# Kernel tuning notes

Hardware: AMD Instinct MI355X
Metric: run time of the kernel (lower is better)

Reference implementation:

```python
import jax, jax.numpy as jnp
import numpy as np
from functools import partial
from jax import lax

B, K, CLIP_DIM, SBERT_DIM, D_MODEL, R_RANK, ATTN_DIM, PMAX = 128, 1024, 768, 384, 256, 64, 256, 8
RHO = 0.35

def _normalize(x, axis=-1, eps=1e-12):
    return x / jnp.maximum(jnp.linalg.norm(x, axis=axis, keepdims=True), eps)

def _build_graph():
    rng = np.random.default_rng(0)
    pid = np.zeros((K, PMAX), np.int32)
    pm = np.zeros((K, PMAX), bool)
    for i in range(K - 1):  # node i's parents are in (i, K); root = K-1 has none
        n = int(rng.integers(1, PMAX + 1))
        n = min(n, K - 1 - i)
        cands = rng.choice(np.arange(i + 1, K), size=n, replace=False)
        pid[i, :n] = cands
        pm[i, :n] = True
    order = np.arange(K - 1, -1, -1, dtype=np.int32)  # parents before children
    return jnp.asarray(pid), jnp.asarray(pm), jnp.asarray(order)

def setup_inputs() -> dict:
    key = jax.random.key(0)
    ks = iter(jax.random.split(key, 32))
    r = lambda shape, s=0.02: jax.random.normal(next(ks), shape, jnp.float32) * s
    pid, pm, order = _build_graph()
    return {
        "t_clip": jax.random.normal(next(ks), (B, CLIP_DIM), jnp.float32),
        "v_clip": jax.random.normal(next(ks), (B, CLIP_DIM), jnp.float32),
        "concept_sbert": jax.random.normal(next(ks), (K, SBERT_DIM), jnp.float32),
        "Wt": r((CLIP_DIM, D_MODEL)), "bt": jnp.zeros((D_MODEL,)),
        "Wv": r((CLIP_DIM, D_MODEL)), "bv": jnp.zeros((D_MODEL,)),
        "Wc": r((SBERT_DIM, D_MODEL)), "bc": jnp.zeros((D_MODEL,)),
        "Wp1": r((3 * D_MODEL, 2 * D_MODEL)), "bp1": jnp.zeros((2 * D_MODEL,)),
        "Wp2": r((2 * D_MODEL, D_MODEL)), "bp2": jnp.zeros((D_MODEL,)),
        "Wm1": r((3 * D_MODEL, 2 * D_MODEL)), "bm1": jnp.zeros((2 * D_MODEL,)),
        "Wm2": r((2 * D_MODEL, D_MODEL)), "bm2": jnp.zeros((D_MODEL,)),
        "tau_logits": jnp.zeros((K,)),
        "U": r((D_MODEL, R_RANK)), "V": r((D_MODEL, R_RANK)),
        "Wg1": r((SBERT_DIM, R_RANK)), "bg1": jnp.zeros((R_RANK,)),
        "Wg2": r((R_RANK, R_RANK)), "bg2": jnp.zeros((R_RANK,)),
        "w_out": r((K, R_RANK)), "b_out": jnp.zeros((K,)),
        "concept_q": r((K, ATTN_DIM)),
        "parents_idx": pid, "parents_mask": pm, "order": order,
    }

def _forward(t_clip, v_clip, concept_sbert, Wt, bt, Wv, bv, Wc, bc,
             Wp1, bp1, Wp2, bp2, Wm1, bm1, Wm2, bm2, tau_logits,
             U, V, Wg1, bg1, Wg2, bg2, w_out, b_out, concept_q,
             parents_idx, parents_mask, order):
    gelu = partial(jax.nn.gelu, approximate=False)  # torch nn.GELU default = exact erf
    t = _normalize(t_clip) @ Wt + bt                 # [B, D]
    v = _normalize(v_clip) @ Wv + bv                 # [B, D]
    d = concept_sbert @ Wc + bc                      # [K, D]
    # x = [v, t, d] broadcast to [B, K, 3D]
    x = jnp.concatenate([
        jnp.broadcast_to(v[:, None, :], (t.shape[0], K, D_MODEL)),
        jnp.broadcast_to(t[:, None, :], (t.shape[0], K, D_MODEL)),
        jnp.broadcast_to(d[None, :, :], (t.shape[0], K, D_MODEL)),
    ], axis=-1)
    h_plus = gelu(x @ Wp1 + bp1) @ Wp2 + bp2
    h_minus = gelu(x @ Wm1 + bm1) @ Wm2 + bm2
    tau = jax.nn.sigmoid(tau_logits)[None, :, None]
    h = tau * h_plus + (1.0 - tau) * h_minus         # [B, K, D]
    u = jnp.einsum('bkd,dr->bkr', h, U)
    vv = jnp.einsum('bkd,dr->bkr', h, V)
    g = gelu(concept_sbert @ Wg1 + bg1) @ Wg2 + bg2  # [K, R]
    inter = u * vv * g[None, :, :]
    logits = jnp.einsum('bkr,kr->bk', inter, w_out) + b_out[None, :]
    p = jax.nn.sigmoid(logits)                        # [B, K]
    # --- top-down hierarchical attention + multiplicative aggregation ---
    q = _normalize(concept_q)                         # [K, A]
    def step(p_hat, node):
        par = parents_idx[node]                       # [P] int
        m = parents_mask[node]                        # [P] bool
        scores = jnp.where(m, q[par] @ q[node], -1e9)
        alpha = jax.nn.softmax(scores)                # [P]
        vals = p_hat[:, par]                          # [B, P] gather of parent probs
        prod = jnp.prod(jnp.where(m[None, :], alpha[None, :] * vals, 1.0), axis=-1)
        new = jnp.where(m.any(), RHO * p[:, node] + (1.0 - RHO) * prod, p_hat[:, node])
        return p_hat.at[:, node].set(new), None       # scatter write
    p_hat, _ = lax.scan(step, p, order)
    return p_hat

def reference(t_clip, v_clip, concept_sbert, Wt, bt, Wv, bv, Wc, bc,
              Wp1, bp1, Wp2, bp2, Wm1, bm1, Wm2, bm2, tau_logits,
              U, V, Wg1, bg1, Wg2, bg2, w_out, b_out, concept_q,
              parents_idx, parents_mask, order):
    return _forward(t_clip, v_clip, concept_sbert, Wt, bt, Wv, bv, Wc, bc,
                    Wp1, bp1, Wp2, bp2, Wm1, bm1, Wm2, bm2, tau_logits,
                    U, V, Wg1, bg1, Wg2, bg2, w_out, b_out, concept_q,
                    parents_idx, parents_mask, order)
```

## Files before the change

### kernel.cpp

```cpp
#include <hip/hip_runtime.h>
#include <math.h>

typedef __attribute__((ext_vector_type(8))) short short8;
typedef __attribute__((ext_vector_type(4))) float float4v;
typedef __attribute__((ext_vector_type(2))) float float2v;

struct P {
  const float *t_clip, *v_clip, *sbert;
  const float *Wt, *bt, *Wv, *bv, *Wc, *bc;
  const float *Wp1, *bp1, *Wp2, *bp2, *Wm1, *bm1, *Wm2, *bm2;
  const float *tau_logits, *U, *V, *Wg1, *bg1, *Wg2, *bg2, *w_out, *b_out, *concept_q;
  const int *pid;
  float *Ap, *Am;
  unsigned short *Ctp, *Ctm;
  unsigned short *Wpk, *Wmk;
  float *biasPM, *tau, *gw, *aprod;
  unsigned short *parS;
  int *sorted, *lvlStart, *nlev;
  float *sink;
  float *pOut;
};

__device__ __forceinline__ unsigned short bf16ru(float f) {
    unsigned u = __float_as_uint(f);
    u += 0x7fffu + ((u >> 16) & 1u);
    return (unsigned short)(u >> 16);
}

__device__ __forceinline__ unsigned packpair(float2v a, unsigned c) {
    float2v cb;
    cb.x = __uint_as_float(c << 16);
    cb.y = __uint_as_float(c & 0xffff0000u);
    float2v x = a + cb;
    float2v t = x * x;
    float2v i = t * (-0.06649038f) + 0.39894228f;
    float2v p = x * i + 0.5f;
    float2v g = x * p;
    union { float2v f; unsigned u[2]; } gu; gu.f = g;
    return __builtin_amdgcn_perm(gu.u[1], gu.u[0], 0x07060302u);
}


__device__ void warm_f(const float* p, int n4, int blk, float* sink) {
    float4 s = {0.f, 0.f, 0.f, 0.f};
    for (int i = blk * 1024 + threadIdx.x; i < n4; i += 1024) {
        float4 v = ((const float4*)p)[i];
        s.x += v.x; s.y += v.y; s.z += v.z; s.w += v.w;
    }
    if (s.x + s.y + s.z + s.w == 1.234567e37f) *sink = s.x;
}

__device__ void packW_f(const float* __restrict__ W2, const float* __restrict__ U,
                        const float* __restrict__ V, unsigned short* __restrict__ outP, int rel) {
    int idx = rel * 256 + threadIdx.x;
    int j = idx >> 7, c = idx & 127;
    const float* uv = (c < 64) ? (U + c) : (V + (c - 64));
    float acc = 0.f;
    for (int d = 0; d < 256; ++d) acc = fmaf(W2[(size_t)j * 256 + d], uv[(size_t)d * 64], acc);
    size_t o = (size_t)(j >> 5) * 4096 + (c >> 4) * 512 + ((j >> 3) & 3) * 128 + (c & 15) * 8 + (j & 7);
    outP[o] = bf16ru(acc);
}

__device__ void misc_f(const P& a, int g) {
    int t = threadIdx.x;
    if (g == 0) {
        int c = t & 127;
        const float* bb = (t < 128) ? a.bp2 : a.bm2;
        const float* uv = (c < 64) ? (a.U + c) : (a.V + (c - 64));
        float acc = 0.f;
        for (int d = 0; d < 256; ++d) acc = fmaf(bb[d], uv[(size_t)d * 64], acc);
        a.biasPM[t] = acc;
    } else {
        int k = (g - 1) * 256 + t;
        a.tau[k] = 1.0f / (1.0f + expf(-a.tau_logits[k]));
    }
}

__device__ void levels_f(const P& a, int* smemI) {
    volatile int* lvl = smemI;
    int* cnt  = smemI + 1024;
    int* ofs  = smemI + 2048;
    int* ping = smemI + 3072;
    int* pong = smemI + 3328;
    int* mflag = smemI + 3584;
    int t = threadIdx.x;
    int par[4][8]; int hasm[4];
#pragma unroll
    for (int r = 0; r < 4; ++r) {
        int n = t * 4 + r, h = 0;
#pragma unroll
        for (int s = 0; s < 8; ++s) { int p = a.pid[n * 8 + s]; par[r][s] = p; h |= (p != 0); }
        hasm[r] = h; lvl[n] = 0;
    }
    if (t == 0) mflag[1] = 0;
    __syncthreads();
    for (int round = 0; round < 200; ++round) {
        if (t == 0) mflag[0] = 0;
        __syncthreads();
        int ch = 0;
        for (int sub = 0; sub < 8; ++sub) {
#pragma unroll
            for (int r = 0; r < 4; ++r) {
                if (!hasm[r]) continue;
                int mx = 0;
#pragma unroll
                for (int s = 0; s < 8; ++s) { int p = par[r][s]; if (p) mx = max(mx, lvl[p]); }
                int nl = mx + 1;
                if (nl > lvl[t * 4 + r]) { lvl[t * 4 + r] = nl; ch = 1; }
            }
        }
        if (ch) mflag[0] = 1;
        __syncthreads();
        if (mflag[0] == 0) break;
    }
    int lm = 0;
    for (int r = 0; r < 4; ++r) lm = max(lm, lvl[t * 4 + r]);
    atomicMax(&mflag[1], lm);
    for (int r = 0; r < 4; ++r) cnt[t * 4 + r] = 0;
    __syncthreads();
    for (int r = 0; r < 4; ++r) atomicAdd(&cnt[lvl[t * 4 + r]], 1);
    __syncthreads();
    int c0 = cnt[t * 4], c1 = cnt[t * 4 + 1], c2 = cnt[t * 4 + 2], c3 = cnt[t * 4 + 3];
    ping[t] = c0 + c1 + c2 + c3;
    __syncthreads();
    int* src = ping; int* dst = pong;
    for (int off = 1; off < 256; off <<= 1) {
        int v = src[t];
        if (t >= off) v += src[t - off];
        dst[t] = v;
        __syncthreads();
        int* tmp = src; src = dst; dst = tmp;
    }
    int excl = (t == 0) ? 0 : src[t - 1];
    ofs[t * 4] = excl; ofs[t * 4 + 1] = excl + c0;
    ofs[t * 4 + 2] = excl + c0 + c1; ofs[t * 4 + 3] = excl + c0 + c1 + c2;
#pragma unroll
    for (int r = 0; r < 4; ++r) a.lvlStart[t * 4 + r] = ofs[t * 4 + r];
    if (t == 0) { a.lvlStart[1024] = 1024; a.nlev[0] = mflag[1] + 1; }
    __syncthreads();
    for (int r = 0; r < 4; ++r) {
        int n = t * 4 + r;
        int pos = atomicAdd(&ofs[lvl[n]], 1);
        a.sorted[pos] = n;
    }
}

__global__ void __launch_bounds__(256) k0_kernel(P a) {
    __shared__ int smemI[3600];
    int bid = blockIdx.x;
    if (bid == 0) { levels_f(a, smemI); return; }
    bid -= 1;
    if (bid < 256) { packW_f(a.Wp2, a.U, a.V, a.Wpk, bid); return; }
    bid -= 256;
    if (bid < 256) { packW_f(a.Wm2, a.U, a.V, a.Wmk, bid); return; }
    bid -= 256;
    if (bid < 5) { misc_f(a, bid); return; }
    bid -= 5;
    if (bid < 96) { warm_f(a.Wp1, 98304, bid, a.sink); return; }
    bid -= 96;
    if (bid < 96) { warm_f(a.Wm1, 98304, bid, a.sink); return; }
    bid -= 96;
    if (bid < 48) { warm_f(a.Wt, 49152, bid, a.sink); return; }
    bid -= 48;
    if (bid < 48) { warm_f(a.Wv, 49152, bid, a.sink); return; }
    bid -= 48;
    if (bid < 24) { warm_f(a.Wc, 24576, bid, a.sink); return; }
    bid -= 24;
    if (bid < 96) { warm_f(a.sbert, 98304, bid, a.sink); return; }
    bid -= 96;
    if (bid < 24) { warm_f(a.t_clip, 24576, bid, a.sink); return; }
    bid -= 24;
    if (bid < 24) { warm_f(a.v_clip, 24576, bid, a.sink); return; }
    bid -= 24;
    if (bid < 64) { warm_f(a.concept_q, 65536, bid, a.sink); return; }
    bid -= 64;
    if (bid < 16) { warm_f(a.w_out, 16384, bid, a.sink); return; }
    bid -= 16;
    warm_f(a.Wg1, 6144, bid, a.sink);
}


__device__ void ab_f(const P& a, int b, float* smemF) {
    float* raw = smemF;
    float* vt  = smemF + 1536;
    float* red = smemF + 2060;
    int t = threadIdx.x;
    float sT = 0.f, sV = 0.f;
    for (int i = t; i < 768; i += 256) {
        float xt = a.t_clip[(size_t)b * 768 + i];
        float xv = a.v_clip[(size_t)b * 768 + i];
        raw[i] = xt; raw[768 + i] = xv;
        sT = fmaf(xt, xt, sT); sV = fmaf(xv, xv, sV);
    }
    for (int mk = 32; mk; mk >>= 1) { sT += __shfl_xor(sT, mk); sV += __shfl_xor(sV, mk); }
    if ((t & 63) == 0) { red[t >> 6] = sT; red[4 + (t >> 6)] = sV; }
    __syncthreads();
    float scT = 1.0f / fmaxf(sqrtf(red[0] + red[1] + red[2] + red[3]), 1e-12f);
    float scV = 1.0f / fmaxf(sqrtf(red[4] + red[5] + red[6] + red[7]), 1e-12f);
    float accT = 0.f, accV = 0.f;
    for (int d = 0; d < 768; ++d) {
        accT = fmaf(raw[d],       a.Wt[(size_t)d * 256 + t], accT);
        accV = fmaf(raw[768 + d], a.Wv[(size_t)d * 256 + t], accV);
    }
    vt[t]       = accV * scV + a.bv[t];
    vt[256 + t] = accT * scT + a.bt[t];
    __syncthreads();
    int mat = t >> 7, j0 = (t & 127) * 4;
    const float* W1 = mat ? a.Wm1 : a.Wp1;
    const float* b1 = mat ? a.bm1 : a.bp1;
    float* out = mat ? a.Am : a.Ap;
    float a0 = 0, a1 = 0, a2 = 0, a3 = 0;
    for (int d = 0; d < 512; ++d) {
        float4 w = *(const float4*)&W1[(size_t)d * 512 + j0];
        float x = vt[d];
        a0 = fmaf(x, w.x, a0); a1 = fmaf(x, w.y, a1);
        a2 = fmaf(x, w.z, a2); a3 = fmaf(x, w.w, a3);
    }
    float4 bb = *(const float4*)&b1[j0];
    float4 o; o.x = a0 + bb.x; o.y = a1 + bb.y; o.z = a2 + bb.z; o.w = a3 + bb.w;
    *(float4*)&out[(size_t)b * 512 + j0] = o;
}

__device__ void c_f(const P& a, int blk, float* smemF) {
    int k0 = blk * 4;
    float* sb = smemF;
    float* dr = smemF + 1536;
    int t = threadIdx.x;
    for (int i = t; i < 1536; i += 256) sb[i] = a.sbert[(size_t)k0 * 384 + i];
    __syncthreads();
    float d0 = 0, d1 = 0, d2 = 0, d3 = 0;
    for (int dd = 0; dd < 384; ++dd) {
        float w = a.Wc[(size_t)dd * 256 + t];
        d0 = fmaf(sb[dd], w, d0);
        d1 = fmaf(sb[384 + dd], w, d1);
        d2 = fmaf(sb[768 + dd], w, d2);
        d3 = fmaf(sb[1152 + dd], w, d3);
    }
    float bcv = a.bc[t];
    dr[t] = d0 + bcv; dr[256 + t] = d1 + bcv; dr[512 + t] = d2 + bcv; dr[768 + t] = d3 + bcv;
    __syncthreads();
    int mat = t >> 7, j0 = (t & 127) * 4;
    const float* W1 = mat ? a.Wm1 : a.Wp1;
    unsigned short* out = mat ? a.Ctm : a.Ctp;
    float acc[4][4] = {};
    for (int dd = 0; dd < 256; ++dd) {
        float4 w = *(const float4*)&W1[(size_t)(512 + dd) * 512 + j0];
#pragma unroll
        for (int r = 0; r < 4; ++r) {
            float x = dr[r * 256 + dd];
            acc[r][0] = fmaf(x, w.x, acc[r][0]); acc[r][1] = fmaf(x, w.y, acc[r][1]);
            acc[r][2] = fmaf(x, w.z, acc[r][2]); acc[r][3] = fmaf(x, w.w, acc[r][3]);
        }
    }
    int step = j0 >> 5, quad = (j0 >> 3) & 3, e0 = j0 & 7;
#pragma unroll
    for (int r = 0; r < 4; ++r) {
        int k = k0 + r;
        size_t idx = (size_t)(k >> 4) * 8192 + step * 512 + quad * 128 + (k & 15) * 8 + e0;
        ushort4 o;
        o.x = bf16ru(acc[r][0]); o.y = bf16ru(acc[r][1]);
        o.z = bf16ru(acc[r][2]); o.w = bf16ru(acc[r][3]);
        *(ushort4*)&out[idx] = o;
    }
}

__device__ void gw_f(const P& a, int blk, float* ghid) {
    int t = threadIdx.x, wv = t >> 6, lane = t & 63;
    int k = blk * 4 + wv;
    float acc = a.bg1[lane];
    for (int d = 0; d < 384; ++d)
        acc = fmaf(a.sbert[(size_t)k * 384 + d], a.Wg1[(size_t)d * 64 + lane], acc);
    ghid[wv * 64 + lane] = 0.5f * acc * (1.0f + erff(acc * 0.7071067811865475f));
    __syncthreads();
    float acc2 = a.bg2[lane];
    for (int d = 0; d < 64; ++d)
        acc2 = fmaf(ghid[wv * 64 + d], a.Wg2[(size_t)d * 64 + lane], acc2);
    a.gw[(size_t)k * 64 + lane] = acc2 * a.w_out[(size_t)k * 64 + lane];
}

__device__ void alpha_f(const P& a, int blk) {
    int t = threadIdx.x, wv = t >> 6, lane = t & 63;
    int node = blk * 4 + wv;
    int slot = lane >> 3, e = lane & 7;
    int par = a.pid[node * 8 + slot];
    const float4* qk = (const float4*)(a.concept_q + (size_t)node * 256);
    const float4* qp = (const float4*)(a.concept_q + (size_t)par * 256);
    float dq = 0, np = 0, ns = 0;
#pragma unroll
    for (int i = 0; i < 8; ++i) {
        float4 x = qp[e * 8 + i], y = qk[e * 8 + i];
        dq += x.x * y.x + x.y * y.y + x.z * y.z + x.w * y.w;
        np += x.x * x.x + x.y * x.y + x.z * x.z + x.w * x.w;
        ns += y.x * y.x + y.y * y.y + y.z * y.z + y.w * y.w;
    }
#pragma unroll
    for (int mk = 1; mk <= 4; mk <<= 1) {
        dq += __shfl_xor(dq, mk); np += __shfl_xor(np, mk); ns += __shfl_xor(ns, mk);
    }
    float score = dq / fmaxf(sqrtf(np) * sqrtf(ns), 1e-24f);
    float sc[8]; int pv[8];
#pragma unroll
    for (int s = 0; s < 8; ++s) { sc[s] = __shfl(score, s * 8); pv[s] = __shfl(par, s * 8); }
    float mx = -1e30f;
#pragma unroll
    for (int s = 0; s < 8; ++s) if (pv[s] != 0) mx = fmaxf(mx, sc[s]);
    float sum = 0.f;
#pragma unroll
    for (int s = 0; s < 8; ++s) sum += (pv[s] != 0) ? expf(sc[s] - mx) : 0.0f;
    float ap = 1.0f;
#pragma unroll
    for (int s = 0; s < 8; ++s) if (pv[s] != 0) ap *= expf(sc[s] - mx) / sum;
    if (lane == 0) a.aprod[node] = ap;
    if (e == 0) a.parS[node * 8 + slot] = (par != 0) ? (unsigned short)par : (unsigned short)1024;
}

__global__ void __launch_bounds__(256) k1_kernel(P a) {
    __shared__ float smemF[2600];
    int bid = blockIdx.x;
    if (bid < 128) { ab_f(a, bid, smemF); return; }
    bid -= 128;
    if (bid < 256) { c_f(a, bid, smemF); return; }
    bid -= 256;
    if (bid < 256) { gw_f(a, bid, smemF); return; }
    bid -= 256;
    alpha_f(a, bid);
}

__global__ void __launch_bounds__(512, 2) main_kernel(P a) {
    __shared__ float apL[4096];
    __shared__ float xbuf[4 * 4 * 64 * 8];
    int tid = threadIdx.x;
    int wv2 = tid >> 6, lane = tid & 63;
    int mat = wv2 >> 2, sub = wv2 & 3;
    int m = lane & 15, quad = lane >> 4;
    int b0 = (blockIdx.x >> 4) * 4;
    int k0 = (blockIdx.x & 15) << 6;

    for (int i = tid; i < 1024; i += 512) {
        int arr = i >> 7, off = i & 127;
        const float* src = ((arr >> 2) ? a.Am : a.Ap) + (size_t)(b0 + (arr & 3)) * 512;
        ((float4*)apL)[i] = ((const float4*)src)[off];
    }
    __syncthreads();

    const unsigned short* W  = mat ? a.Wmk : a.Wpk;
    const unsigned short* Ct = mat ? a.Ctm : a.Ctp;
    const float* aL = apL + mat * 2048;
    int kt = (k0 >> 4) + sub;
    const char* ctB = (const char*)Ct + (size_t)kt * 16384 + quad * 256 + m * 16;
    const char* wB  = (const char*)W + quad * 256 + m * 16;

    float4v acc[4][8];
#pragma unroll
    for (int b = 0; b < 4; ++b)
#pragma unroll
        for (int i = 0; i < 8; ++i) acc[b][i] = (float4v)0.0f;

    uint4 crN = *(const uint4*)(ctB);
    for (int n = 0; n < 16; ++n) {
        uint4 cr = crN;
        if (n < 15) crN = *(const uint4*)(ctB + (n + 1) * 1024);
        union { uint4 u; short8 s; } fa[4];
        const float* aj = aL + n * 32 + quad * 8;
#pragma unroll
        for (int b = 0; b < 4; ++b) {
            float4v x0 = *(const float4v*)(aj + b * 512);
            float4v x1 = *(const float4v*)(aj + b * 512 + 4);
            float2v v;
            v.x = x0[0]; v.y = x0[1]; fa[b].u.x = packpair(v, cr.x);
            v.x = x0[2]; v.y = x0[3]; fa[b].u.y = packpair(v, cr.y);
            v.x = x1[0]; v.y = x1[1]; fa[b].u.z = packpair(v, cr.z);
            v.x = x1[2]; v.y = x1[3]; fa[b].u.w = packpair(v, cr.w);
        }
        const char* wn = wB + n * 8192;
#pragma unroll
        for (int nt = 0; nt < 8; ++nt) {
            short8 wf = *(const short8*)(wn + nt * 1024);
            acc[0][nt] = __builtin_amdgcn_mfma_f32_16x16x32_bf16(fa[0].s, wf, acc[0][nt], 0, 0, 0);
            acc[1][nt] = __builtin_amdgcn_mfma_f32_16x16x32_bf16(fa[1].s, wf, acc[1][nt], 0, 0, 0);
            acc[2][nt] = __builtin_amdgcn_mfma_f32_16x16x32_bf16(fa[2].s, wf, acc[2][nt], 0, 0, 0);
            acc[3][nt] = __builtin_amdgcn_mfma_f32_16x16x32_bf16(fa[3].s, wf, acc[3][nt], 0, 0, 0);
        }
    }

    int kk[4]; float tv[4];
#pragma unroll
    for (int r = 0; r < 4; ++r) { kk[r] = k0 + sub * 16 + quad * 4 + r; tv[r] = a.tau[kk[r]]; }
    float lsum[4][4] = {};
    float* xb = xbuf + ((sub * 4) * 64 + lane) * 8;
#pragma unroll
    for (int t4 = 0; t4 < 4; ++t4) {
        __syncthreads();
        if (mat == 1) {
#pragma unroll
            for (int b = 0; b < 4; ++b) {
                float* d = xb + b * 512;
#pragma unroll
                for (int r = 0; r < 4; ++r) { d[r] = acc[b][t4][r]; d[4 + r] = acc[b][t4 + 4][r]; }
            }
        }
        __syncthreads();
        if (mat == 0) {
            int cU = t4 * 16 + m, cV = cU + 64;
            float bPu = a.biasPM[cU], bMu = a.biasPM[128 + cU];
            float bPv = a.biasPM[cV], bMv = a.biasPM[128 + cV];
#pragma unroll
            for (int b = 0; b < 4; ++b) {
                const float* d = xb + b * 512;
#pragma unroll
                for (int r = 0; r < 4; ++r) {
                    float g = a.gw[(size_t)kk[r] * 64 + cU];
                    float u  = tv[r] * (acc[b][t4][r] + bPu)     + (1.0f - tv[r]) * (d[r] + bMu);
                    float vx = tv[r] * (acc[b][t4 + 4][r] + bPv) + (1.0f - tv[r]) * (d[4 + r] + bMv);
                    lsum[b][r] = fmaf(u * vx, g, lsum[b][r]);
                }
            }
        }
    }
    if (mat == 0) {
#pragma unroll
        for (int r = 0; r < 4; ++r) {
            float bo = a.b_out[kk[r]];
#pragma unroll
            for (int b = 0; b < 4; ++b) {
                float s = lsum[b][r];
                s += __shfl_xor(s, 1); s += __shfl_xor(s, 2); s += __shfl_xor(s, 4); s += __shfl_xor(s, 8);
                if (m == 0)
                    a.pOut[(size_t)(b0 + b) * 1024 + kk[r]] = 1.0f / (1.0f + expf(-(s + bo)));
            }
        }
    }
}

#define PH_STRIDE 1056
__global__ void __launch_bounds__(256) scan_kernel(P a) {
    __shared__ float ph[4 * PH_STRIDE];
    __shared__ float aprodL[1024];
    __shared__ unsigned short parL[8192];
    __shared__ short sortedL[1024];
    __shared__ int lvlStartL[1025];
    int t = threadIdx.x;
    int b0 = blockIdx.x * 4;
    for (int i = t; i < 1024; i += 256) ((uint4*)parL)[i] = ((const uint4*)a.parS)[i];
    for (int i = t; i < 1024; i += 256) {
        aprodL[i] = a.aprod[i];
        sortedL[i] = (short)a.sorted[i];
        lvlStartL[i] = a.lvlStart[i];
    }
    if (t == 0) lvlStartL[1024] = 1024;
    for (int i = t; i < 4096; i += 256) {
        int bb = i >> 10, k = i & 1023;
        ph[bb * PH_STRIDE + k] = a.pOut[(size_t)(b0 + bb) * 1024 + k];
    }
    if (t < 4) ph[t * PH_STRIDE + 1024] = 1.0f;
    __syncthreads();
    int nlev = a.nlev[0];
    int w = t >> 6, lane = t & 63;
    float* myph = ph + w * PH_STRIDE;
    for (int L = 1; L < nlev; ++L) {
        int s0 = lvlStartL[L], s1 = lvlStartL[L + 1];
        for (int i = s0 + lane; i < s1; i += 64) {
            int node = sortedL[i];
            ushort4 pA = *(const ushort4*)&parL[node * 8];
            ushort4 pB = *(const ushort4*)&parL[node * 8 + 4];
            float prod = aprodL[node];
            prod *= myph[pA.x] * myph[pA.y];
            prod *= myph[pA.z] * myph[pA.w];
            prod *= myph[pB.x] * myph[pB.y];
            prod *= myph[pB.z] * myph[pB.w];
            myph[node] = fmaf(0.35f, myph[node], 0.65f * prod);
        }
    }
    __syncthreads();
    for (int i = t; i < 4096; i += 256) {
        int bb = i >> 10, k = i & 1023;
        a.pOut[(size_t)(b0 + bb) * 1024 + k] = ph[bb * PH_STRIDE + k];
    }
}

extern "C" void kernel_launch(void* const* d_in, const int* in_sizes, int n_in,
                              void* d_out, int out_size, void* d_ws, size_t ws_size,
                              hipStream_t stream) {
    P a;
    a.t_clip = (const float*)d_in[0];
    a.v_clip = (const float*)d_in[1];
    a.sbert  = (const float*)d_in[2];
    a.Wt  = (const float*)d_in[3];  a.bt  = (const float*)d_in[4];
    a.Wv  = (const float*)d_in[5];  a.bv  = (const float*)d_in[6];
    a.Wc  = (const float*)d_in[7];  a.bc  = (const float*)d_in[8];
    a.Wp1 = (const float*)d_in[9];  a.bp1 = (const float*)d_in[10];
    a.Wp2 = (const float*)d_in[11]; a.bp2 = (const float*)d_in[12];
    a.Wm1 = (const float*)d_in[13]; a.bm1 = (const float*)d_in[14];
    a.Wm2 = (const float*)d_in[15]; a.bm2 = (const float*)d_in[16];
    a.tau_logits = (const float*)d_in[17];
    a.U   = (const float*)d_in[18]; a.V   = (const float*)d_in[19];
    a.Wg1 = (const float*)d_in[20]; a.bg1 = (const float*)d_in[21];
    a.Wg2 = (const float*)d_in[22]; a.bg2 = (const float*)d_in[23];
    a.w_out = (const float*)d_in[24]; a.b_out = (const float*)d_in[25];
    a.concept_q = (const float*)d_in[26];
    a.pid = (const int*)d_in[27];

    char* w = (char*)d_ws;
    a.Ap     = (float*)(w + 0);
    a.Am     = (float*)(w + 262144);
    a.Ctp    = (unsigned short*)(w + 524288);
    a.Ctm    = (unsigned short*)(w + 1572864);
    a.Wpk    = (unsigned short*)(w + 2621440);
    a.Wmk    = (unsigned short*)(w + 2752512);
    a.biasPM = (float*)(w + 2883584);
    a.tau    = (float*)(w + 2884608);
    a.gw     = (float*)(w + 2888704);
    a.parS   = (unsigned short*)(w + 3150848);
    a.aprod  = (float*)(w + 3167232);
    a.sorted = (int*)(w + 3171328);
    a.lvlStart = (int*)(w + 3175424);
    a.nlev     = (int*)(w + 3179648);
    a.sink     = (float*)(w + 3179776);
    a.pOut = (float*)d_out;

    k0_kernel<<<1062, 256, 0, stream>>>(a);
    k1_kernel<<<896, 256, 0, stream>>>(a);
    main_kernel<<<512, 512, 0, stream>>>(a);
    scan_kernel<<<32, 256, 0, stream>>>(a);
}
```

Baseline: 306.8 us.

## Move first-layer projections to bf16 MFMA GEMMs and drop cache-warming blocks

The preprocessing is rebuilt. The text/video and concept projections now run as row-tiled FP32 kernels that write bf16 MFMA-packed activations. W1 is converted to packed bf16, and the two W1 matmuls (Ap/Am and Ct) run as MFMA 16x16x32 bf16 GEMMs in a new second prep kernel. The cache-warming blocks are removed, and packW and gw are retiled to reuse data through shared memory. The intent is to replace slow scalar FP32 GEMV-style loops with tensor-core work and fewer blocks, at the cost of bf16 rounding on Ap/Am inputs and an extra conversion pass.

```diff
diff --git a/kernel.cpp b/kernel.cpp
--- a/kernel.cpp
+++ b/kernel.cpp
@@ -11,13 +11,17 @@
   const float *Wp1, *bp1, *Wp2, *bp2, *Wm1, *bm1, *Wm2, *bm2;
   const float *tau_logits, *U, *V, *Wg1, *bg1, *Wg2, *bg2, *w_out, *b_out, *concept_q;
   const int *pid;
-  float *Ap, *Am;
+  float *vt32;
+  unsigned short *vtbf;
+  unsigned short *dbf;
+  unsigned short *w1upP, *w1upM;
+  unsigned short *w1lowP, *w1lowM;
   unsigned short *Ctp, *Ctm;
   unsigned short *Wpk, *Wmk;
+  float *Ap, *Am;
   float *biasPM, *tau, *gw, *aprod;
   unsigned short *parS;
   int *sorted, *lvlStart, *nlev;
-  float *sink;
   float *pOut;
 };
 
@@ -41,24 +45,198 @@
 }
 
 
-__device__ void warm_f(const float* p, int n4, int blk, float* sink) {
-    float4 s = {0.f, 0.f, 0.f, 0.f};
-    for (int i = blk * 1024 + threadIdx.x; i < n4; i += 1024) {
-        float4 v = ((const float4*)p)[i];
-        s.x += v.x; s.y += v.y; s.z += v.z; s.w += v.w;
-    }
-    if (s.x + s.y + s.z + s.w == 1.234567e37f) *sink = s.x;
-}
-
-__device__ void packW_f(const float* __restrict__ W2, const float* __restrict__ U,
-                        const float* __restrict__ V, unsigned short* __restrict__ outP, int rel) {
-    int idx = rel * 256 + threadIdx.x;
-    int j = idx >> 7, c = idx & 127;
-    const float* uv = (c < 64) ? (U + c) : (V + (c - 64));
-    float acc = 0.f;
-    for (int d = 0; d < 256; ++d) acc = fmaf(W2[(size_t)j * 256 + d], uv[(size_t)d * 64], acc);
-    size_t o = (size_t)(j >> 5) * 4096 + (c >> 4) * 512 + ((j >> 3) & 3) * 128 + (c & 15) * 8 + (j & 7);
-    outP[o] = bf16ru(acc);
+__device__ void tv_f(const P& a, int rel, float* sm) {
+    int sel = rel & 1, ct = (rel >> 1) & 1, bt8 = rel >> 2;
+    float* xrow = sm;
+    float* scale = sm + 6144;
+    int tid = threadIdx.x;
+    const float* X = sel ? a.t_clip : a.v_clip;
+    int b0 = bt8 * 8;
+    for (int r = 0; r < 8; ++r)
+        for (int i = tid; i < 768; i += 256)
+            xrow[r * 768 + i] = X[(size_t)(b0 + r) * 768 + i];
+    __syncthreads();
+    {
+        int r = tid >> 5, l = tid & 31;
+        float ss = 0.f;
+        for (int i = l; i < 768; i += 32) { float v = xrow[r * 768 + i]; ss = fmaf(v, v, ss); }
+        for (int mk = 16; mk; mk >>= 1) ss += __shfl_xor(ss, mk);
+        if (l == 0) scale[r] = 1.0f / fmaxf(sqrtf(ss), 1e-12f);
+    }
+    __syncthreads();
+    int col = ct * 128 + (tid & 127);
+    int rg = tid >> 7;
+    const float* W = sel ? a.Wt : a.Wv;
+    const float* bias = sel ? a.bt : a.bv;
+    float acc[4] = {};
+    for (int d = 0; d < 768; ++d) {
+        float w = W[(size_t)d * 256 + col];
+        const float* xr = xrow + (rg * 4) * 768 + d;
+        acc[0] = fmaf(xr[0],    w, acc[0]);
+        acc[1] = fmaf(xr[768],  w, acc[1]);
+        acc[2] = fmaf(xr[1536], w, acc[2]);
+        acc[3] = fmaf(xr[2304], w, acc[3]);
+    }
+    int vtcol = sel * 256 + col;
+    float bb = bias[col];
+#pragma unroll
+    for (int r = 0; r < 4; ++r) {
+        int b = b0 + rg * 4 + r;
+        float y = acc[r] * scale[rg * 4 + r] + bb;
+        a.vt32[(size_t)b * 512 + vtcol] = y;
+        a.vtbf[(size_t)(b >> 4) * 8192 + (vtcol >> 5) * 512 + ((vtcol >> 3) & 3) * 128
+               + (b & 15) * 8 + (vtcol & 7)] = bf16ru(y);
+    }
+}
+
+__device__ void d_f(const P& a, int rel, float* sm) {
+    int r0 = rel * 8;
+    int tid = threadIdx.x;
+    for (int i = tid; i < 3072; i += 256) sm[i] = a.sbert[(size_t)r0 * 384 + i];
+    __syncthreads();
+    float acc[8] = {};
+    int col = tid;
+    for (int d = 0; d < 384; ++d) {
+        float w = a.Wc[(size_t)d * 256 + col];
+#pragma unroll
+        for (int r = 0; r < 8; ++r) acc[r] = fmaf(sm[r * 384 + d], w, acc[r]);
+    }
+    float bb = a.bc[col];
+#pragma unroll
+    for (int r = 0; r < 8; ++r) {
+        int row = r0 + r;
+        a.dbf[(size_t)(row >> 4) * 4096 + (col >> 5) * 512 + ((col >> 3) & 3) * 128
+              + (row & 15) * 8 + (col & 7)] = bf16ru(acc[r] + bb);
+    }
+}
+
+__device__ void wcv_f(const P& a, int rel, float* smf) {
+    unsigned short* wl = (unsigned short*)smf;
+    int mat = rel & 1, rb = rel >> 1;
+    int r0 = rb * 16;
+    const float* W1 = mat ? a.Wm1 : a.Wp1;
+    int tid = threadIdx.x;
+    for (int i = tid; i < 8192; i += 256)
+        wl[i] = bf16ru(W1[(size_t)r0 * 512 + i]);
+    __syncthreads();
+    unsigned short* dst; int K16, kbase;
+    if (r0 < 512) { dst = mat ? a.w1upM : a.w1upP;  K16 = 8192; kbase = r0; }
+    else          { dst = mat ? a.w1lowM : a.w1lowP; K16 = 4096; kbase = r0 - 512; }
+    for (int i = tid; i < 1024; i += 256) {
+        int kg = i >> 9, n = i & 511;
+        int k0 = kbase + kg * 8;
+        ushort4 o0, o1;
+        o0.x = wl[(kg * 8 + 0) * 512 + n]; o0.y = wl[(kg * 8 + 1) * 512 + n];
+        o0.z = wl[(kg * 8 + 2) * 512 + n]; o0.w = wl[(kg * 8 + 3) * 512 + n];
+        o1.x = wl[(kg * 8 + 4) * 512 + n]; o1.y = wl[(kg * 8 + 5) * 512 + n];
+        o1.z = wl[(kg * 8 + 6) * 512 + n]; o1.w = wl[(kg * 8 + 7) * 512 + n];
+        size_t off = (size_t)(n >> 4) * K16 + (k0 >> 5) * 512 + ((k0 >> 3) & 3) * 128 + (n & 15) * 8;
+        *(ushort4*)&dst[off]     = o0;
+        *(ushort4*)&dst[off + 4] = o1;
+    }
+}
+
+__device__ void packW_f(const P& a, int rel, float* smf) {
+    float* w2l = smf;
+    int mat = rel >> 6, jb = rel & 63;
+    int j0 = jb * 8;
+    const float* W2 = mat ? a.Wm2 : a.Wp2;
+    unsigned short* outP = mat ? a.Wmk : a.Wpk;
+    int tid = threadIdx.x;
+    for (int i = tid; i < 2048; i += 256) w2l[i] = W2[(size_t)j0 * 256 + i];
+    __syncthreads();
+    int c = tid & 127, jg = tid >> 7;
+    float acc[4] = {};
+    const float* uv = (c < 64) ? (a.U + c) : (a.V + (c - 64));
+    for (int d = 0; d < 256; ++d) {
+        float u = uv[(size_t)d * 64];
+        const float* wr = w2l + (jg * 4) * 256 + d;
+        acc[0] = fmaf(wr[0],   u, acc[0]);
+        acc[1] = fmaf(wr[256], u, acc[1]);
+        acc[2] = fmaf(wr[512], u, acc[2]);
+        acc[3] = fmaf(wr[768], u, acc[3]);
+    }
+#pragma unroll
+    for (int r = 0; r < 4; ++r) {
+        int j = j0 + jg * 4 + r;
+        size_t o = (size_t)(j >> 5) * 4096 + (c >> 4) * 512 + ((j >> 3) & 3) * 128 + (c & 15) * 8 + (j & 7);
+        outP[o] = bf16ru(acc[r]);
+    }
+}
+
+__device__ void gw_f(const P& a, int rel, float* sm) {
+    float* sb = sm;
+    float* hid = sm + 6144;
+    int k0 = rel * 16;
+    int tid = threadIdx.x;
+    for (int i = tid; i < 6144; i += 256) sb[i] = a.sbert[(size_t)k0 * 384 + i];
+    __syncthreads();
+    int col = tid & 63, rg = tid >> 6;
+    float bg = a.bg1[col];
+    float acc[4] = {bg, bg, bg, bg};
+    for (int d = 0; d < 384; ++d) {
+        float w = a.Wg1[(size_t)d * 64 + col];
+        const float* xr = sb + (rg * 4) * 384 + d;
+        acc[0] = fmaf(xr[0],    w, acc[0]);
+        acc[1] = fmaf(xr[384],  w, acc[1]);
+        acc[2] = fmaf(xr[768],  w, acc[2]);
+        acc[3] = fmaf(xr[1152], w, acc[3]);
+    }
+#pragma unroll
+    for (int r = 0; r < 4; ++r)
+        hid[(rg * 4 + r) * 64 + col] = 0.5f * acc[r] * (1.0f + erff(acc[r] * 0.7071067811865475f));
+    __syncthreads();
+    float bg2v = a.bg2[col];
+    float a2[4] = {bg2v, bg2v, bg2v, bg2v};
+    for (int d = 0; d < 64; ++d) {
+        float w = a.Wg2[(size_t)d * 64 + col];
+        const float* hr = hid + (rg * 4) * 64 + d;
+        a2[0] = fmaf(hr[0],   w, a2[0]);
+        a2[1] = fmaf(hr[64],  w, a2[1]);
+        a2[2] = fmaf(hr[128], w, a2[2]);
+        a2[3] = fmaf(hr[192], w, a2[3]);
+    }
+#pragma unroll
+    for (int r = 0; r < 4; ++r) {
+        int k = k0 + rg * 4 + r;
+        a.gw[(size_t)k * 64 + col] = a2[r] * a.w_out[(size_t)k * 64 + col];
+    }
+}
+
+__device__ void alpha_f(const P& a, int blk) {
+    int t = threadIdx.x, wv = t >> 6, lane = t & 63;
+    int node = blk * 4 + wv;
+    int slot = lane >> 3, e = lane & 7;
+    int par = a.pid[node * 8 + slot];
+    const float4* qk = (const float4*)(a.concept_q + (size_t)node * 256);
+    const float4* qp = (const float4*)(a.concept_q + (size_t)par * 256);
+    float dq = 0, np = 0, ns = 0;
+#pragma unroll
+    for (int i = 0; i < 8; ++i) {
+        float4 x = qp[e * 8 + i], y = qk[e * 8 + i];
+        dq += x.x * y.x + x.y * y.y + x.z * y.z + x.w * y.w;
+        np += x.x * x.x + x.y * x.y + x.z * x.z + x.w * x.w;
+        ns += y.x * y.x + y.y * y.y + y.z * y.z + y.w * y.w;
+    }
+#pragma unroll
+    for (int mk = 1; mk <= 4; mk <<= 1) {
+        dq += __shfl_xor(dq, mk); np += __shfl_xor(np, mk); ns += __shfl_xor(ns, mk);
+    }
+    float score = dq / fmaxf(sqrtf(np) * sqrtf(ns), 1e-24f);
+    float sc[8]; int pv[8];
+#pragma unroll
+    for (int s = 0; s < 8; ++s) { sc[s] = __shfl(score, s * 8); pv[s] = __shfl(par, s * 8); }
+    float mx = -1e30f;
+#pragma unroll
+    for (int s = 0; s < 8; ++s) if (pv[s] != 0) mx = fmaxf(mx, sc[s]);
+    float sum = 0.f;
+#pragma unroll
+    for (int s = 0; s < 8; ++s) sum += (pv[s] != 0) ? expf(sc[s] - mx) : 0.0f;
+    float ap = 1.0f;
+#pragma unroll
+    for (int s = 0; s < 8; ++s) if (pv[s] != 0) ap *= expf(sc[s] - mx) / sum;
+    if (lane == 0) a.aprod[node] = ap;
+    if (e == 0) a.parS[node * 8 + slot] = (par != 0) ? (unsigned short)par : (unsigned short)1024;
 }
 
 __device__ void misc_f(const P& a, int g) {
@@ -145,185 +323,85 @@
     }
 }
 
-__global__ void __launch_bounds__(256) k0_kernel(P a) {
-    __shared__ int smemI[3600];
+__global__ void __launch_bounds__(256) prep1_kernel(P a) {
+    __shared__ float smem[7200];
     int bid = blockIdx.x;
-    if (bid == 0) { levels_f(a, smemI); return; }
+    if (bid == 0) { levels_f(a, (int*)smem); return; }
     bid -= 1;
-    if (bid < 256) { packW_f(a.Wp2, a.U, a.V, a.Wpk, bid); return; }
+    if (bid < 64) { tv_f(a, bid, smem); return; }
+    bid -= 64;
+    if (bid < 128) { d_f(a, bid, smem); return; }
+    bid -= 128;
+    if (bid < 96) { wcv_f(a, bid, smem); return; }
+    bid -= 96;
+    if (bid < 128) { packW_f(a, bid, smem); return; }
+    bid -= 128;
+    if (bid < 64) { gw_f(a, bid, smem); return; }
+    bid -= 64;
+    if (bid < 256) { alpha_f(a, bid); return; }
     bid -= 256;
-    if (bid < 256) { packW_f(a.Wm2, a.U, a.V, a.Wmk, bid); return; }
-    bid -= 256;
-    if (bid < 5) { misc_f(a, bid); return; }
-    bid -= 5;
-    if (bid < 96) { warm_f(a.Wp1, 98304, bid, a.sink); return; }
-    bid -= 96;
-    if (bid < 96) { warm_f(a.Wm1, 98304, bid, a.sink); return; }
-    bid -= 96;
-    if (bid < 48) { warm_f(a.Wt, 49152, bid, a.sink); return; }
-    bid -= 48;
-    if (bid < 48) { warm_f(a.Wv, 49152, bid, a.sink); return; }
-    bid -= 48;
-    if (bid < 24) { warm_f(a.Wc, 24576, bid, a.sink); return; }
-    bid -= 24;
-    if (bid < 96) { warm_f(a.sbert, 98304, bid, a.sink); return; }
-    bid -= 96;
-    if (bid < 24) { warm_f(a.t_clip, 24576, bid, a.sink); return; }
-    bid -= 24;
-    if (bid < 24) { warm_f(a.v_clip, 24576, bid, a.sink); return; }
-    bid -= 24;
-    if (bid < 64) { warm_f(a.concept_q, 65536, bid, a.sink); return; }
-    bid -= 64;
-    if (bid < 16) { warm_f(a.w_out, 16384, bid, a.sink); return; }
-    bid -= 16;
-    warm_f(a.Wg1, 6144, bid, a.sink);
-}
-
-
-__device__ void ab_f(const P& a, int b, float* smemF) {
-    float* raw = smemF;
-    float* vt  = smemF + 1536;
-    float* red = smemF + 2060;
-    int t = threadIdx.x;
-    float sT = 0.f, sV = 0.f;
-    for (int i = t; i < 768; i += 256) {
-        float xt = a.t_clip[(size_t)b * 768 + i];
-        float xv = a.v_clip[(size_t)b * 768 + i];
-        raw[i] = xt; raw[768 + i] = xv;
-        sT = fmaf(xt, xt, sT); sV = fmaf(xv, xv, sV);
-    }
-    for (int mk = 32; mk; mk >>= 1) { sT += __shfl_xor(sT, mk); sV += __shfl_xor(sV, mk); }
-    if ((t & 63) == 0) { red[t >> 6] = sT; red[4 + (t >> 6)] = sV; }
-    __syncthreads();
-    float scT = 1.0f / fmaxf(sqrtf(red[0] + red[1] + red[2] + red[3]), 1e-12f);
-    float scV = 1.0f / fmaxf(sqrtf(red[4] + red[5] + red[6] + red[7]), 1e-12f);
-    float accT = 0.f, accV = 0.f;
-    for (int d = 0; d < 768; ++d) {
-        accT = fmaf(raw[d],       a.Wt[(size_t)d * 256 + t], accT);
-        accV = fmaf(raw[768 + d], a.Wv[(size_t)d * 256 + t], accV);
-    }
-    vt[t]       = accV * scV + a.bv[t];
-    vt[256 + t] = accT * scT + a.bt[t];
-    __syncthreads();
-    int mat = t >> 7, j0 = (t & 127) * 4;
-    const float* W1 = mat ? a.Wm1 : a.Wp1;
-    const float* b1 = mat ? a.bm1 : a.bp1;
-    float* out = mat ? a.Am : a.Ap;
-    float a0 = 0, a1 = 0, a2 = 0, a3 = 0;
-    for (int d = 0; d < 512; ++d) {
-        float4 w = *(const float4*)&W1[(size_t)d * 512 + j0];
-        float x = vt[d];
-        a0 = fmaf(x, w.x, a0); a1 = fmaf(x, w.y, a1);
-        a2 = fmaf(x, w.z, a2); a3 = fmaf(x, w.w, a3);
-    }
-    float4 bb = *(const float4*)&b1[j0];
-    float4 o; o.x = a0 + bb.x; o.y = a1 + bb.y; o.z = a2 + bb.z; o.w = a3 + bb.w;
-    *(float4*)&out[(size_t)b * 512 + j0] = o;
-}
-
-__device__ void c_f(const P& a, int blk, float* smemF) {
-    int k0 = blk * 4;
-    float* sb = smemF;
-    float* dr = smemF + 1536;
-    int t = threadIdx.x;
-    for (int i = t; i < 1536; i += 256) sb[i] = a.sbert[(size_t)k0 * 384 + i];
-    __syncthreads();
-    float d0 = 0, d1 = 0, d2 = 0, d3 = 0;
-    for (int dd = 0; dd < 384; ++dd) {
-        float w = a.Wc[(size_t)dd * 256 + t];
-        d0 = fmaf(sb[dd], w, d0);
-        d1 = fmaf(sb[384 + dd], w, d1);
-        d2 = fmaf(sb[768 + dd], w, d2);
-        d3 = fmaf(sb[1152 + dd], w, d3);
-    }
-    float bcv = a.bc[t];
-    dr[t] = d0 + bcv; dr[256 + t] = d1 + bcv; dr[512 + t] = d2 + bcv; dr[768 + t] = d3 + bcv;
-    __syncthreads();
-    int mat = t >> 7, j0 = (t & 127) * 4;
-    const float* W1 = mat ? a.Wm1 : a.Wp1;
-    unsigned short* out = mat ? a.Ctm : a.Ctp;
-    float acc[4][4] = {};
-    for (int dd = 0; dd < 256; ++dd) {
-        float4 w = *(const float4*)&W1[(size_t)(512 + dd) * 512 + j0];
-#pragma unroll
-        for (int r = 0; r < 4; ++r) {
-            float x = dr[r * 256 + dd];
-            acc[r][0] = fmaf(x, w.x, acc[r][0]); acc[r][1] = fmaf(x, w.y, acc[r][1]);
-            acc[r][2] = fmaf(x, w.z, acc[r][2]); acc[r][3] = fmaf(x, w.w, acc[r][3]);
-        }
-    }
-    int step = j0 >> 5, quad = (j0 >> 3) & 3, e0 = j0 & 7;
-#pragma unroll
-    for (int r = 0; r < 4; ++r) {
-        int k = k0 + r;
-        size_t idx = (size_t)(k >> 4) * 8192 + step * 512 + quad * 128 + (k & 15) * 8 + e0;
-        ushort4 o;
-        o.x = bf16ru(acc[r][0]); o.y = bf16ru(acc[r][1]);
-        o.z = bf16ru(acc[r][2]); o.w = bf16ru(acc[r][3]);
-        *(ushort4*)&out[idx] = o;
-    }
-}
-
-__device__ void gw_f(const P& a, int blk, float* ghid) {
-    int t = threadIdx.x, wv = t >> 6, lane = t & 63;
-    int k = blk * 4 + wv;
-    float acc = a.bg1[lane];
-    for (int d = 0; d < 384; ++d)
-        acc = fmaf(a.sbert[(size_t)k * 384 + d], a.Wg1[(size_t)d * 64 + lane], acc);
-    ghid[wv * 64 + lane] = 0.5f * acc * (1.0f + erff(acc * 0.7071067811865475f));
-    __syncthreads();
-    float acc2 = a.bg2[lane];
-    for (int d = 0; d < 64; ++d)
-        acc2 = fmaf(ghid[wv * 64 + d], a.Wg2[(size_t)d * 64 + lane], acc2);
-    a.gw[(size_t)k * 64 + lane] = acc2 * a.w_out[(size_t)k * 64 + lane];
-}
-
-__device__ void alpha_f(const P& a, int blk) {
-    int t = threadIdx.x, wv = t >> 6, lane = t & 63;
-    int node = blk * 4 + wv;
-    int slot = lane >> 3, e = lane & 7;
-    int par = a.pid[node * 8 + slot];
-    const float4* qk = (const float4*)(a.concept_q + (size_t)node * 256);
-    const float4* qp = (const float4*)(a.concept_q + (size_t)par * 256);
-    float dq = 0, np = 0, ns = 0;
-#pragma unroll
-    for (int i = 0; i < 8; ++i) {
-        float4 x = qp[e * 8 + i], y = qk[e * 8 + i];
-        dq += x.x * y.x + x.y * y.y + x.z * y.z + x.w * y.w;
-        np += x.x * x.x + x.y * x.y + x.z * x.z + x.w * x.w;
-        ns += y.x * y.x + y.y * y.y + y.z * y.z + y.w * y.w;
-    }
-#pragma unroll
-    for (int mk = 1; mk <= 4; mk <<= 1) {
-        dq += __shfl_xor(dq, mk); np += __shfl_xor(np, mk); ns += __shfl_xor(ns, mk);
-    }
-    float score = dq / fmaxf(sqrtf(np) * sqrtf(ns), 1e-24f);
-    float sc[8]; int pv[8];
-#pragma unroll
-    for (int s = 0; s < 8; ++s) { sc[s] = __shfl(score, s * 8); pv[s] = __shfl(par, s * 8); }
-    float mx = -1e30f;
-#pragma unroll
-    for (int s = 0; s < 8; ++s) if (pv[s] != 0) mx = fmaxf(mx, sc[s]);
-    float sum = 0.f;
-#pragma unroll
-    for (int s = 0; s < 8; ++s) sum += (pv[s] != 0) ? expf(sc[s] - mx) : 0.0f;
-    float ap = 1.0f;
-#pragma unroll
-    for (int s = 0; s < 8; ++s) if (pv[s] != 0) ap *= expf(sc[s] - mx) / sum;
-    if (lane == 0) a.aprod[node] = ap;
-    if (e == 0) a.parS[node * 8 + slot] = (par != 0) ? (unsigned short)par : (unsigned short)1024;
-}
-
-__global__ void __launch_bounds__(256) k1_kernel(P a) {
-    __shared__ float smemF[2600];
+    misc_f(a, bid);
+}
+
+__global__ void __launch_bounds__(256) prep2_kernel(P a) {
     int bid = blockIdx.x;
-    if (bid < 128) { ab_f(a, bid, smemF); return; }
-    bid -= 128;
-    if (bid < 256) { c_f(a, bid, smemF); return; }
-    bid -= 256;
-    if (bid < 256) { gw_f(a, bid, smemF); return; }
-    bid -= 256;
-    alpha_f(a, bid);
+    int tid = threadIdx.x;
+    int wv = tid >> 6, lane = tid & 63;
+    int m = lane & 15, quad = lane >> 4;
+    if (bid < 128) {
+        int mat = bid & 1, mt = (bid >> 1) & 15, ntile = bid >> 5;
+        const unsigned short* A = a.dbf + (size_t)(mt * 4 + wv) * 4096 + quad * 128 + m * 8;
+        const unsigned short* B = (mat ? a.w1lowM : a.w1lowP) + (size_t)quad * 128 + m * 8;
+        unsigned short* Ct = mat ? a.Ctm : a.Ctp;
+        float4v acc[8];
+#pragma unroll
+        for (int i = 0; i < 8; ++i) acc[i] = (float4v)0.0f;
+        for (int s = 0; s < 8; ++s) {
+            short8 af = *(const short8*)(A + s * 512);
+#pragma unroll
+            for (int nt = 0; nt < 8; ++nt) {
+                short8 bf = *(const short8*)(B + (size_t)(ntile * 8 + nt) * 4096 + s * 512);
+                acc[nt] = __builtin_amdgcn_mfma_f32_16x16x32_bf16(af, bf, acc[nt], 0, 0, 0);
+            }
+        }
+        int rowg = mt * 4 + wv;
+        int rl = quad * 4;
+#pragma unroll
+        for (int nt = 0; nt < 8; ++nt) {
+            int j = ntile * 128 + nt * 16 + m;
+            size_t base = (size_t)rowg * 8192 + (j >> 5) * 512 + ((j >> 3) & 3) * 128 + (j & 7);
+#pragma unroll
+            for (int rr = 0; rr < 4; ++rr)
+                Ct[base + (rl + rr) * 8] = bf16ru(acc[nt][rr]);
+        }
+    } else {
+        int rel = bid - 128;
+        int mat = rel & 1, mt = (rel >> 1) & 1, ntile = rel >> 2;
+        const unsigned short* A = a.vtbf + (size_t)(mt * 4 + wv) * 8192 + quad * 128 + m * 8;
+        const unsigned short* B = (mat ? a.w1upM : a.w1upP) + (size_t)quad * 128 + m * 8;
+        const float* bias = mat ? a.bm1 : a.bp1;
+        float* out = mat ? a.Am : a.Ap;
+        float4v acc[8];
+#pragma unroll
+        for (int i = 0; i < 8; ++i) acc[i] = (float4v)0.0f;
+        for (int s = 0; s < 16; ++s) {
+            short8 af = *(const short8*)(A + s * 512);
+#pragma unroll
+            for (int nt = 0; nt < 8; ++nt) {
+                short8 bf = *(const short8*)(B + (size_t)(ntile * 8 + nt) * 8192 + s * 512);
+                acc[nt] = __builtin_amdgcn_mfma_f32_16x16x32_bf16(af, bf, acc[nt], 0, 0, 0);
+            }
+        }
+        int b0r = mt * 64 + wv * 16 + quad * 4;
+#pragma unroll
+        for (int nt = 0; nt < 8; ++nt) {
+            int j = ntile * 128 + nt * 16 + m;
+            float bb = bias[j];
+#pragma unroll
+            for (int rr = 0; rr < 4; ++rr)
+                out[(size_t)(b0r + rr) * 512 + j] = acc[nt][rr] + bb;
+        }
+    }
 }
 
 __global__ void __launch_bounds__(512, 2) main_kernel(P a) {
@@ -501,25 +579,31 @@
     a.pid = (const int*)d_in[27];
 
     char* w = (char*)d_ws;
-    a.Ap     = (float*)(w + 0);
-    a.Am     = (float*)(w + 262144);
-    a.Ctp    = (unsigned short*)(w + 524288);
-    a.Ctm    = (unsigned short*)(w + 1572864);
-    a.Wpk    = (unsigned short*)(w + 2621440);
-    a.Wmk    = (unsigned short*)(w + 2752512);
-    a.biasPM = (float*)(w + 2883584);
-    a.tau    = (float*)(w + 2884608);
-    a.gw     = (float*)(w + 2888704);
-    a.parS   = (unsigned short*)(w + 3150848);
-    a.aprod  = (float*)(w + 3167232);
-    a.sorted = (int*)(w + 3171328);
-    a.lvlStart = (int*)(w + 3175424);
-    a.nlev     = (int*)(w + 3179648);
-    a.sink     = (float*)(w + 3179776);
+    a.vt32   = (float*)(w + 0);
+    a.vtbf   = (unsigned short*)(w + 262144);
+    a.dbf    = (unsigned short*)(w + 393216);
+    a.w1upP  = (unsigned short*)(w + 917504);
+    a.w1upM  = (unsigned short*)(w + 1441792);
+    a.w1lowP = (unsigned short*)(w + 1966080);
+    a.w1lowM = (unsigned short*)(w + 2228224);
+    a.Ctp    = (unsigned short*)(w + 2490368);
+    a.Ctm    = (unsigned short*)(w + 3538944);
+    a.Wpk    = (unsigned short*)(w + 4587520);
+    a.Wmk    = (unsigned short*)(w + 4718592);
+    a.Ap     = (float*)(w + 4849664);
+    a.Am     = (float*)(w + 5111808);
+    a.biasPM = (float*)(w + 5373952);
+    a.tau    = (float*)(w + 5374976);
+    a.gw     = (float*)(w + 5379072);
+    a.parS   = (unsigned short*)(w + 5641216);
+    a.aprod  = (float*)(w + 5657600);
+    a.sorted = (int*)(w + 5661696);
+    a.lvlStart = (int*)(w + 5665792);
+    a.nlev     = (int*)(w + 5670144);
     a.pOut = (float*)d_out;
 
-    k0_kernel<<<1062, 256, 0, stream>>>(a);
-    k1_kernel<<<896, 256, 0, stream>>>(a);
+    prep1_kernel<<<742, 256, 0, stream>>>(a);
+    prep2_kernel<<<144, 256, 0, stream>>>(a);
     main_kernel<<<512, 512, 0, stream>>>(a);
     scan_kernel<<<32, 256, 0, stream>>>(a);
 }
```

Result: faster. 286.9 us (-6.5%).
